# Optimization experiments

Hardware: AMD Instinct MI355X
Metric: run time of the kernel (lower is better)

Reference implementation:

```python
import jax, jax.numpy as jnp
import numpy as np

B = 256          # graphs per batch
N = 128          # nodes per graph (equal-size graphs; batch is block-contiguous)
P = N * (N - 1) // 2  # pairs per graph = 8128
E = B * 1024     # total edges
D = 128          # node feature dim
L = 32           # latent dim

# precomputed local upper-triangular pair indices (constants)
_PI, _PJ = np.triu_indices(N, k=1)
_PI = jnp.asarray(_PI); _PJ = jnp.asarray(_PJ)


def setup_inputs() -> dict:
    key = jax.random.key(0)
    ks = jax.random.split(key, 8)
    x = jax.random.normal(ks[0], (B * N, D), dtype=jnp.float32)
    # within-graph edges with local i < j
    li = jax.random.randint(ks[1], (E,), 0, N - 1)
    r = jax.random.randint(ks[2], (E,), 0, 1 << 30)
    lj = li + 1 + r % (N - 1 - li)
    g = jax.random.randint(ks[3], (E,), 0, B)
    off = g * N
    edge_index = jnp.stack([off + li, off + lj]).astype(jnp.int64)
    batch = jnp.repeat(jnp.arange(B), N).astype(jnp.int64)
    eps = jax.random.normal(ks[4], (B * N, L), dtype=jnp.float32)
    W1 = jax.random.normal(ks[5], (D, D), dtype=jnp.float32) * 0.05
    b1 = jnp.zeros((D,), dtype=jnp.float32)
    Wmu = jax.random.normal(ks[6], (D, L), dtype=jnp.float32) * 0.05
    bmu = jnp.zeros((L,), dtype=jnp.float32)
    Wls = jax.random.normal(ks[7], (D, L), dtype=jnp.float32) * 0.05
    bls = jnp.zeros((L,), dtype=jnp.float32)
    return {"x": x, "edge_index": edge_index, "batch": batch, "eps": eps,
            "W1": W1, "b1": b1, "Wmu": Wmu, "bmu": bmu, "Wls": Wls, "bls": bls}


def reference(x, edge_index, batch, eps, W1, b1, Wmu, bmu, Wls, bls):
    src, dst = edge_index[0], edge_index[1]
    # --- encoder: one symmetric message-passing layer -> Gaussian q per node ---
    agg = jnp.zeros_like(x).at[dst].add(x[src]).at[src].add(x[dst])
    h = jax.nn.relu((x + agg) @ W1 + b1)
    mu = h @ Wmu + bmu                       # [BN, L]
    log_std = h @ Wls + bls
    std = jnp.exp(log_std)
    z = mu + std * eps                       # rsample
    # --- KL(q || N(0,I)) per node, summed per graph (kls[b]) ---
    kl_node = 0.5 * jnp.sum(std * std + mu * mu - 1.0 - 2.0 * log_std, axis=-1)
    kls = jax.ops.segment_sum(kl_node, batch, num_segments=B)  # [B]
    # --- link targets: scatter edges into triangular pair slots ---
    li, lj, be = src % N, dst % N, src // N
    pidx = li * (2 * N - li - 1) // 2 + (lj - li - 1)
    targets = jnp.zeros((B, P), dtype=z.dtype).at[be, pidx].set(1.0)
    # --- inner-product Bernoulli decoder over all pairs of every graph ---
    zb = z.reshape(B, N, L)
    logits = jnp.einsum('bpl,bpl->bp', zb[:, _PI], zb[:, _PJ])   # [B, P]
    log_probs = jnp.sum(targets * logits - jax.nn.softplus(logits), axis=-1)  # [B]
    elbo = jnp.mean(log_probs - kls)
    return -elbo
```

## Files before the change

kernel.cpp:

```cpp
#include <hip/hip_runtime.h>
#include <math.h>

#define B_ 256
#define N_ 128
#define D_ 128
#define L_ 32
#define E_ 262144
#define PW_ 254
#define DCAP 96

#define NDEG_OFF 0
#define BM_OFF   32768
#define KLS_OFF  97792
#define LP_OFF   98048
#define ADJ_OFF  98304
#define Z_OFF    884736
#define ZERO_WORDS 98304

__global__ __launch_bounds__(256) void k_build(
    const int* __restrict__ ei, unsigned* __restrict__ ndeg,
    unsigned char* __restrict__ adj, unsigned* __restrict__ bm)
{
    int e = blockIdx.x * 256 + threadIdx.x;
    int src = ei[e], dst = ei[E_ + e];
    unsigned s1 = atomicAdd(&ndeg[src], 1u);
    if (s1 < DCAP) adj[(size_t)src * DCAP + s1] = (unsigned char)(dst & 127);
    unsigned s2 = atomicAdd(&ndeg[dst], 1u);
    if (s2 < DCAP) adj[(size_t)dst * DCAP + s2] = (unsigned char)(src & 127);
    int li = src & 127, lj = dst & 127, g = src >> 7;
    int p = li * (255 - li) / 2 + (lj - li - 1);
    atomicOr(&bm[g * PW_ + (p >> 5)], 1u << (p & 31));
}

__global__ __launch_bounds__(256, 4) void k_encoder(
    const float* __restrict__ x, const unsigned* __restrict__ ndeg,
    const unsigned char* __restrict__ adj,
    const float* __restrict__ W1, const float* __restrict__ b1,
    const float* __restrict__ Wmu, const float* __restrict__ bmu,
    const float* __restrict__ Wls, const float* __restrict__ bls,
    const float* __restrict__ eps,
    float* __restrict__ z, float* __restrict__ kls)
{
    __shared__ float XAs[32 * 132];
    __shared__ float Ws[4096];
    __shared__ float RED[256];
    int t = threadIdx.x;
    int g = blockIdx.x & 255;
    int quar = blockIdx.x >> 8;
    int row0 = g * 128 + quar * 32;
    int rg = t >> 5;
    int cg = t & 31;

    {
        int nidx = t >> 4;
        int fo = (t & 15) * 8;
        for (int p = 0; p < 2; ++p) {
            int lrow = p * 16 + nidx;
            int gnode = row0 + lrow;
            const float* xr = x + (size_t)gnode * 128 + fo;
            float4 a0 = *(const float4*)xr;
            float4 a1 = *(const float4*)(xr + 4);
            int deg = (int)ndeg[gnode];
            if (deg > DCAP) deg = DCAP;
            const unsigned char* al = adj + (size_t)gnode * DCAP;
            const float* gx = x + (size_t)(gnode & ~127) * 128 + fo;
            int e = 0;
            for (; e + 4 <= deg; e += 4) {
                unsigned pk = *(const unsigned*)(al + e);
                const float* r0 = gx + (pk & 255u) * 128;
                const float* r1 = gx + ((pk >> 8) & 255u) * 128;
                const float* r2 = gx + ((pk >> 16) & 255u) * 128;
                const float* r3 = gx + (pk >> 24) * 128;
                float4 v00 = *(const float4*)r0, v01 = *(const float4*)(r0 + 4);
                float4 v10 = *(const float4*)r1, v11 = *(const float4*)(r1 + 4);
                float4 v20 = *(const float4*)r2, v21 = *(const float4*)(r2 + 4);
                float4 v30 = *(const float4*)r3, v31 = *(const float4*)(r3 + 4);
                a0.x += v00.x + v10.x + v20.x + v30.x;
                a0.y += v00.y + v10.y + v20.y + v30.y;
                a0.z += v00.z + v10.z + v20.z + v30.z;
                a0.w += v00.w + v10.w + v20.w + v30.w;
                a1.x += v01.x + v11.x + v21.x + v31.x;
                a1.y += v01.y + v11.y + v21.y + v31.y;
                a1.z += v01.z + v11.z + v21.z + v31.z;
                a1.w += v01.w + v11.w + v21.w + v31.w;
            }
            for (; e < deg; ++e) {
                const float* r = gx + (unsigned)al[e] * 128;
                float4 v0 = *(const float4*)r, v1 = *(const float4*)(r + 4);
                a0.x += v0.x; a0.y += v0.y; a0.z += v0.z; a0.w += v0.w;
                a1.x += v1.x; a1.y += v1.y; a1.z += v1.z; a1.w += v1.w;
            }
            *(float4*)(XAs + lrow * 132 + fo) = a0;
            *(float4*)(XAs + lrow * 132 + fo + 4) = a1;
        }
    }
    __syncthreads();

    float acc[4][4];
    #pragma unroll
    for (int i = 0; i < 4; ++i)
        #pragma unroll
        for (int j = 0; j < 4; ++j) acc[i][j] = 0.f;

    for (int kq = 0; kq < 4; ++kq) {
        if (kq) __syncthreads();
        #pragma unroll
        for (int i = 0; i < 4; ++i) {
            int c = t + i * 256;
            ((float4*)Ws)[c] = ((const float4*)(W1 + kq * 4096))[c];
        }
        __syncthreads();
        #pragma unroll 2
        for (int k = 0; k < 32; k += 4) {
            float4 av[4], wv[4];
            #pragma unroll
            for (int i = 0; i < 4; ++i)
                av[i] = *(const float4*)(XAs + (4 * rg + i) * 132 + kq * 32 + k);
            #pragma unroll
            for (int dk = 0; dk < 4; ++dk)
                wv[dk] = *(const float4*)(Ws + (k + dk) * 128 + 4 * cg);
            #pragma unroll
            for (int i = 0; i < 4; ++i) {
                acc[i][0] += av[i].x * wv[0].x + av[i].y * wv[1].x + av[i].z * wv[2].x + av[i].w * wv[3].x;
                acc[i][1] += av[i].x * wv[0].y + av[i].y * wv[1].y + av[i].z * wv[2].y + av[i].w * wv[3].y;
                acc[i][2] += av[i].x * wv[0].z + av[i].y * wv[1].z + av[i].z * wv[2].z + av[i].w * wv[3].z;
                acc[i][3] += av[i].x * wv[0].w + av[i].y * wv[1].w + av[i].z * wv[2].w + av[i].w * wv[3].w;
            }
        }
    }
    __syncthreads();

    {
        float4 bb = *(const float4*)(b1 + 4 * cg);
        #pragma unroll
        for (int i = 0; i < 4; ++i) {
            float4 h;
            h.x = fmaxf(acc[i][0] + bb.x, 0.f);
            h.y = fmaxf(acc[i][1] + bb.y, 0.f);
            h.z = fmaxf(acc[i][2] + bb.z, 0.f);
            h.w = fmaxf(acc[i][3] + bb.w, 0.f);
            *(float4*)(XAs + (4 * rg + i) * 132 + 4 * cg) = h;
        }
    }

    float a3[4][2];
    #pragma unroll
    for (int i = 0; i < 4; ++i) { a3[i][0] = 0.f; a3[i][1] = 0.f; }

    for (int kh = 0; kh < 2; ++kh) {
        __syncthreads();
        #pragma unroll
        for (int i = 0; i < 4; ++i) {
            int c = t + i * 256;
            int row = c >> 4, col4 = (c & 15) << 2;
            int rowg = kh * 64 + row;
            float4 v = (col4 < 32) ? *(const float4*)(Wmu + rowg * 32 + col4)
                                   : *(const float4*)(Wls + rowg * 32 + col4 - 32);
            *(float4*)(Ws + row * 64 + col4) = v;
        }
        __syncthreads();
        #pragma unroll 2
        for (int k = 0; k < 64; k += 4) {
            float4 av[4];
            float2 wv[4];
            #pragma unroll
            for (int i = 0; i < 4; ++i)
                av[i] = *(const float4*)(XAs + (4 * rg + i) * 132 + kh * 64 + k);
            #pragma unroll
            for (int dk = 0; dk < 4; ++dk)
                wv[dk] = *(const float2*)(Ws + (k + dk) * 64 + 2 * cg);
            #pragma unroll
            for (int i = 0; i < 4; ++i) {
                a3[i][0] += av[i].x * wv[0].x + av[i].y * wv[1].x + av[i].z * wv[2].x + av[i].w * wv[3].x;
                a3[i][1] += av[i].x * wv[0].y + av[i].y * wv[1].y + av[i].z * wv[2].y + av[i].w * wv[3].y;
            }
        }
    }
    {
        float2 bv = (cg < 16) ? *(const float2*)(bmu + 2 * cg)
                              : *(const float2*)(bls + 2 * cg - 32);
        #pragma unroll
        for (int i = 0; i < 4; ++i) { a3[i][0] += bv.x; a3[i][1] += bv.y; }
    }

    float o3[4][2];
    #pragma unroll
    for (int i = 0; i < 4; ++i) {
        o3[i][0] = __shfl_xor(a3[i][0], 16);
        o3[i][1] = __shfl_xor(a3[i][1], 16);
    }

    float klsum = 0.f;
    if (cg < 16) {
        int lo = cg;
        #pragma unroll
        for (int i = 0; i < 4; ++i) {
            int rowg = row0 + 4 * rg + i;
            float mu0 = a3[i][0], mu1 = a3[i][1];
            float ls0 = o3[i][0], ls1 = o3[i][1];
            float2 ev = *(const float2*)(eps + (size_t)rowg * 32 + 2 * lo);
            float s0 = expf(ls0), s1 = expf(ls1);
            float2 zv = make_float2(mu0 + s0 * ev.x, mu1 + s1 * ev.y);
            *(float2*)(z + (size_t)rowg * 32 + 2 * lo) = zv;
            klsum += s0 * s0 + mu0 * mu0 - 1.f - 2.f * ls0
                   + s1 * s1 + mu1 * mu1 - 1.f - 2.f * ls1;
        }
    }
    RED[t] = klsum;
    __syncthreads();
    for (int s = 128; s > 0; s >>= 1) {
        if (t < s) RED[t] += RED[t + s];
        __syncthreads();
    }
    if (t == 0) atomicAdd(&kls[g], 0.5f * RED[0]);
}

__global__ __launch_bounds__(256) void k_decoder(
    const float* __restrict__ z, const unsigned* __restrict__ bitmap,
    float* __restrict__ logp)
{
    __shared__ float zT[32 * 132];
    __shared__ unsigned bm[PW_];
    __shared__ float RED[256];
    int b = blockIdx.x & 255, quar = blockIdx.x >> 8, t = threadIdx.x;

    #pragma unroll
    for (int i = 0; i < 16; ++i) {
        int c = t + i * 256;
        int n = c >> 5, l = c & 31;
        zT[l * 132 + n] = z[((size_t)b * N_ + n) * L_ + l];
    }
    if (t < PW_) bm[t] = bitmap[b * PW_ + t];
    __syncthreads();

    int i0 = quar * 32 + ((t >> 5) << 2);
    int j0 = (t & 31) << 2;
    float g[4][4];
    #pragma unroll
    for (int a = 0; a < 4; ++a)
        #pragma unroll
        for (int c = 0; c < 4; ++c) g[a][c] = 0.f;

    #pragma unroll 4
    for (int l = 0; l < 32; ++l) {
        float4 a0 = *(const float4*)(zT + l * 132 + i0);
        float4 b0 = *(const float4*)(zT + l * 132 + j0);
        float za[4] = {a0.x, a0.y, a0.z, a0.w};
        float zb[4] = {b0.x, b0.y, b0.z, b0.w};
        #pragma unroll
        for (int a = 0; a < 4; ++a)
            #pragma unroll
            for (int c = 0; c < 4; ++c) g[a][c] += za[a] * zb[c];
    }

    float sum = 0.f;
    #pragma unroll
    for (int a = 0; a < 4; ++a) {
        int i = i0 + a;
        #pragma unroll
        for (int c = 0; c < 4; ++c) {
            int j = j0 + c;
            if (j > i) {
                float lg = g[a][c];
                int p = i * (255 - i) / 2 + (j - i - 1);
                unsigned bit = (bm[p >> 5] >> (p & 31)) & 1u;
                float sp = log1pf(expf(-fabsf(lg))) + fmaxf(lg, 0.f);
                sum += bit ? (lg - sp) : (-sp);
            }
        }
    }
    RED[t] = sum;
    __syncthreads();
    for (int s = 128; s > 0; s >>= 1) {
        if (t < s) RED[t] += RED[t + s];
        __syncthreads();
    }
    if (t == 0) atomicAdd(&logp[b], RED[0]);
}

__global__ __launch_bounds__(256) void k_finalize(
    const float* __restrict__ kls, const float* __restrict__ logp,
    float* __restrict__ out)
{
    __shared__ float RED[256];
    int t = threadIdx.x;
    RED[t] = logp[t] - kls[t];
    __syncthreads();
    for (int s = 128; s > 0; s >>= 1) {
        if (t < s) RED[t] += RED[t + s];
        __syncthreads();
    }
    if (t == 0) out[0] = -RED[0] * (1.0f / 256.0f);
}

extern "C" void kernel_launch(void* const* d_in, const int* in_sizes, int n_in,
                              void* d_out, int out_size, void* d_ws, size_t ws_size,
                              hipStream_t stream) {
    const float* x   = (const float*)d_in[0];
    const int*   ei  = (const int*)d_in[1];
    const float* eps = (const float*)d_in[3];
    const float* W1  = (const float*)d_in[4];
    const float* b1  = (const float*)d_in[5];
    const float* Wmu = (const float*)d_in[6];
    const float* bmu = (const float*)d_in[7];
    const float* Wls = (const float*)d_in[8];
    const float* bls = (const float*)d_in[9];

    unsigned* wsw = (unsigned*)d_ws;
    unsigned*      ndeg = wsw + NDEG_OFF;
    unsigned*      bm   = wsw + BM_OFF;
    float*         kls  = (float*)(wsw + KLS_OFF);
    float*         logp = (float*)(wsw + LP_OFF);
    unsigned char* adj  = (unsigned char*)(wsw + ADJ_OFF);
    float*         z    = (float*)(wsw + Z_OFF);

    hipMemsetAsync(d_ws, 0, ZERO_WORDS * sizeof(unsigned), stream);

    k_build   <<<E_ / 256, 256, 0, stream>>>(ei, ndeg, adj, bm);
    k_encoder <<<1024, 256, 0, stream>>>(x, ndeg, adj, W1, b1, Wmu, bmu,
                                         Wls, bls, eps, z, kls);
    k_decoder <<<4 * B_, 256, 0, stream>>>(z, bm, logp);
    k_finalize<<<1, 256, 0, stream>>>(kls, logp, (float*)d_out);
}
```

Measured before the change: 188.5 us.

## Double-buffer encoder weight tiles, use per-wave rows, fast math, shuffle reductions

The encoder now gives each wave its own 8-row slice of aggregated features. It streams W1 and the mu/log-std weights through double-buffered shared tiles, prefetching the next chunk into registers while computing on the current one, so there are fewer barriers per chunk. Block-level shared-memory tree reductions in the encoder and decoder become wavefront shuffle reductions with one atomic per wave. expf/log1pf are replaced by the __expf/__logf intrinsics, which are cheaper but slightly less accurate, and the per-wave atomics add more atomic traffic.

Measured after the change: 277.8 us. 1.47x slower.

```diff
diff --git a/kernel.cpp b/kernel.cpp
--- a/kernel.cpp
+++ b/kernel.cpp
@@ -41,22 +41,28 @@
     const float* __restrict__ eps,
     float* __restrict__ z, float* __restrict__ kls)
 {
-    __shared__ float XAs[32 * 132];
-    __shared__ float Ws[4096];
-    __shared__ float RED[256];
+    __shared__ float XAW[4][8 * 132];
+    __shared__ float Ws[2][2048];
     int t = threadIdx.x;
     int g = blockIdx.x & 255;
     int quar = blockIdx.x >> 8;
     int row0 = g * 128 + quar * 32;
-    int rg = t >> 5;
-    int cg = t & 31;
+    int w = t >> 6, lane = t & 63;
+    int rg = lane >> 5;
+    int cg = lane & 31;
+    float* myA = XAW[w];
+    int wrow0 = row0 + w * 8;
+
+    float4 wp0 = ((const float4*)W1)[t];
+    float4 wp1 = ((const float4*)W1)[t + 256];
 
     {
-        int nidx = t >> 4;
-        int fo = (t & 15) * 8;
+        int sub = lane >> 4;
+        int fo = (lane & 15) * 8;
+        #pragma unroll 2
         for (int p = 0; p < 2; ++p) {
-            int lrow = p * 16 + nidx;
-            int gnode = row0 + lrow;
+            int lrow = p * 4 + sub;
+            int gnode = wrow0 + lrow;
             const float* xr = x + (size_t)gnode * 128 + fo;
             float4 a0 = *(const float4*)xr;
             float4 a1 = *(const float4*)(xr + 4);
@@ -90,10 +96,12 @@
                 a0.x += v0.x; a0.y += v0.y; a0.z += v0.z; a0.w += v0.w;
                 a1.x += v1.x; a1.y += v1.y; a1.z += v1.z; a1.w += v1.w;
             }
-            *(float4*)(XAs + lrow * 132 + fo) = a0;
-            *(float4*)(XAs + lrow * 132 + fo + 4) = a1;
-        }
-    }
+            *(float4*)(myA + lrow * 132 + fo) = a0;
+            *(float4*)(myA + lrow * 132 + fo + 4) = a1;
+        }
+    }
+    ((float4*)Ws[0])[t] = wp0;
+    ((float4*)Ws[0])[t + 256] = wp1;
     __syncthreads();
 
     float acc[4][4];
@@ -102,23 +110,21 @@
         #pragma unroll
         for (int j = 0; j < 4; ++j) acc[i][j] = 0.f;
 
-    for (int kq = 0; kq < 4; ++kq) {
-        if (kq) __syncthreads();
-        #pragma unroll
-        for (int i = 0; i < 4; ++i) {
-            int c = t + i * 256;
-            ((float4*)Ws)[c] = ((const float4*)(W1 + kq * 4096))[c];
-        }
-        __syncthreads();
-        #pragma unroll 2
-        for (int k = 0; k < 32; k += 4) {
+    for (int c = 0; c < 8; ++c) {
+        if (c < 7) {
+            wp0 = ((const float4*)(W1 + (c + 1) * 2048))[t];
+            wp1 = ((const float4*)(W1 + (c + 1) * 2048))[t + 256];
+        }
+        const float* WsC = Ws[c & 1];
+        #pragma unroll
+        for (int k = 0; k < 16; k += 4) {
             float4 av[4], wv[4];
             #pragma unroll
             for (int i = 0; i < 4; ++i)
-                av[i] = *(const float4*)(XAs + (4 * rg + i) * 132 + kq * 32 + k);
+                av[i] = *(const float4*)(myA + (4 * rg + i) * 132 + c * 16 + k);
             #pragma unroll
             for (int dk = 0; dk < 4; ++dk)
-                wv[dk] = *(const float4*)(Ws + (k + dk) * 128 + 4 * cg);
+                wv[dk] = *(const float4*)(WsC + (k + dk) * 128 + 4 * cg);
             #pragma unroll
             for (int i = 0; i < 4; ++i) {
                 acc[i][0] += av[i].x * wv[0].x + av[i].y * wv[1].x + av[i].z * wv[2].x + av[i].w * wv[3].x;
@@ -127,8 +133,13 @@
                 acc[i][3] += av[i].x * wv[0].w + av[i].y * wv[1].w + av[i].z * wv[2].w + av[i].w * wv[3].w;
             }
         }
-    }
-    __syncthreads();
+        if (c < 7) {
+            float* WsN = Ws[(c + 1) & 1];
+            ((float4*)WsN)[t] = wp0;
+            ((float4*)WsN)[t + 256] = wp1;
+            __syncthreads();
+        }
+    }
 
     {
         float4 bb = *(const float4*)(b1 + 4 * cg);
@@ -139,55 +150,72 @@
             h.y = fmaxf(acc[i][1] + bb.y, 0.f);
             h.z = fmaxf(acc[i][2] + bb.z, 0.f);
             h.w = fmaxf(acc[i][3] + bb.w, 0.f);
-            *(float4*)(XAs + (4 * rg + i) * 132 + 4 * cg) = h;
-        }
-    }
-
-    float a3[4][2];
-    #pragma unroll
-    for (int i = 0; i < 4; ++i) { a3[i][0] = 0.f; a3[i][1] = 0.f; }
-
-    for (int kh = 0; kh < 2; ++kh) {
-        __syncthreads();
-        #pragma unroll
-        for (int i = 0; i < 4; ++i) {
-            int c = t + i * 256;
-            int row = c >> 4, col4 = (c & 15) << 2;
-            int rowg = kh * 64 + row;
-            float4 v = (col4 < 32) ? *(const float4*)(Wmu + rowg * 32 + col4)
-                                   : *(const float4*)(Wls + rowg * 32 + col4 - 32);
-            *(float4*)(Ws + row * 64 + col4) = v;
-        }
-        __syncthreads();
-        #pragma unroll 2
-        for (int k = 0; k < 64; k += 4) {
+            *(float4*)(myA + (4 * rg + i) * 132 + 4 * cg) = h;
+        }
+    }
+
+    {
+        int f0 = t, f1 = t + 256;
+        int r0_ = f0 >> 4, c0_ = (f0 & 15) << 2;
+        int r1_ = f1 >> 4, c1_ = (f1 & 15) << 2;
+        wp0 = (c0_ < 32) ? *(const float4*)(Wmu + r0_ * 32 + c0_)
+                         : *(const float4*)(Wls + r0_ * 32 + c0_ - 32);
+        wp1 = (c1_ < 32) ? *(const float4*)(Wmu + r1_ * 32 + c1_)
+                         : *(const float4*)(Wls + r1_ * 32 + c1_ - 32);
+        ((float4*)Ws[0])[f0] = wp0;
+        ((float4*)Ws[0])[f1] = wp1;
+    }
+    __syncthreads();
+
+    float a2[4][2];
+    #pragma unroll
+    for (int i = 0; i < 4; ++i) { a2[i][0] = 0.f; a2[i][1] = 0.f; }
+
+    for (int q = 0; q < 4; ++q) {
+        if (q < 3) {
+            int f0 = t, f1 = t + 256;
+            int r0_ = (q + 1) * 32 + (f0 >> 4), c0_ = (f0 & 15) << 2;
+            int r1_ = (q + 1) * 32 + (f1 >> 4), c1_ = (f1 & 15) << 2;
+            wp0 = (c0_ < 32) ? *(const float4*)(Wmu + r0_ * 32 + c0_)
+                             : *(const float4*)(Wls + r0_ * 32 + c0_ - 32);
+            wp1 = (c1_ < 32) ? *(const float4*)(Wmu + r1_ * 32 + c1_)
+                             : *(const float4*)(Wls + r1_ * 32 + c1_ - 32);
+        }
+        const float* WsC = Ws[q & 1];
+        #pragma unroll
+        for (int k = 0; k < 32; k += 4) {
             float4 av[4];
             float2 wv[4];
             #pragma unroll
             for (int i = 0; i < 4; ++i)
-                av[i] = *(const float4*)(XAs + (4 * rg + i) * 132 + kh * 64 + k);
+                av[i] = *(const float4*)(myA + (4 * rg + i) * 132 + q * 32 + k);
             #pragma unroll
             for (int dk = 0; dk < 4; ++dk)
-                wv[dk] = *(const float2*)(Ws + (k + dk) * 64 + 2 * cg);
+                wv[dk] = *(const float2*)(WsC + (k + dk) * 64 + 2 * cg);
             #pragma unroll
             for (int i = 0; i < 4; ++i) {
-                a3[i][0] += av[i].x * wv[0].x + av[i].y * wv[1].x + av[i].z * wv[2].x + av[i].w * wv[3].x;
-                a3[i][1] += av[i].x * wv[0].y + av[i].y * wv[1].y + av[i].z * wv[2].y + av[i].w * wv[3].y;
-            }
+                a2[i][0] += av[i].x * wv[0].x + av[i].y * wv[1].x + av[i].z * wv[2].x + av[i].w * wv[3].x;
+                a2[i][1] += av[i].x * wv[0].y + av[i].y * wv[1].y + av[i].z * wv[2].y + av[i].w * wv[3].y;
+            }
+        }
+        if (q < 3) {
+            float* WsN = Ws[(q + 1) & 1];
+            ((float4*)WsN)[t] = wp0;
+            ((float4*)WsN)[t + 256] = wp1;
+            __syncthreads();
         }
     }
     {
-        float2 bv = (cg < 16) ? *(const float2*)(bmu + 2 * cg)
-                              : *(const float2*)(bls + 2 * cg - 32);
-        #pragma unroll
-        for (int i = 0; i < 4; ++i) { a3[i][0] += bv.x; a3[i][1] += bv.y; }
-    }
-
-    float o3[4][2];
+        float2 bv = (cg < 16) ? ((const float2*)bmu)[cg] : ((const float2*)bls)[cg - 16];
+        #pragma unroll
+        for (int i = 0; i < 4; ++i) { a2[i][0] += bv.x; a2[i][1] += bv.y; }
+    }
+
+    float o2[4][2];
     #pragma unroll
     for (int i = 0; i < 4; ++i) {
-        o3[i][0] = __shfl_xor(a3[i][0], 16);
-        o3[i][1] = __shfl_xor(a3[i][1], 16);
+        o2[i][0] = __shfl_xor(a2[i][0], 16);
+        o2[i][1] = __shfl_xor(a2[i][1], 16);
     }
 
     float klsum = 0.f;
@@ -195,24 +223,20 @@
         int lo = cg;
         #pragma unroll
         for (int i = 0; i < 4; ++i) {
-            int rowg = row0 + 4 * rg + i;
-            float mu0 = a3[i][0], mu1 = a3[i][1];
-            float ls0 = o3[i][0], ls1 = o3[i][1];
+            int rowg = wrow0 + 4 * rg + i;
+            float mu0 = a2[i][0], mu1 = a2[i][1];
+            float ls0 = o2[i][0], ls1 = o2[i][1];
             float2 ev = *(const float2*)(eps + (size_t)rowg * 32 + 2 * lo);
-            float s0 = expf(ls0), s1 = expf(ls1);
+            float s0 = __expf(ls0), s1 = __expf(ls1);
             float2 zv = make_float2(mu0 + s0 * ev.x, mu1 + s1 * ev.y);
             *(float2*)(z + (size_t)rowg * 32 + 2 * lo) = zv;
             klsum += s0 * s0 + mu0 * mu0 - 1.f - 2.f * ls0
                    + s1 * s1 + mu1 * mu1 - 1.f - 2.f * ls1;
         }
     }
-    RED[t] = klsum;
-    __syncthreads();
-    for (int s = 128; s > 0; s >>= 1) {
-        if (t < s) RED[t] += RED[t + s];
-        __syncthreads();
-    }
-    if (t == 0) atomicAdd(&kls[g], 0.5f * RED[0]);
+    #pragma unroll
+    for (int off = 32; off > 0; off >>= 1) klsum += __shfl_xor(klsum, off);
+    if (lane == 0) atomicAdd(&kls[g], 0.5f * klsum);
 }
 
 __global__ __launch_bounds__(256) void k_decoder(
@@ -221,7 +245,6 @@
 {
     __shared__ float zT[32 * 132];
     __shared__ unsigned bm[PW_];
-    __shared__ float RED[256];
     int b = blockIdx.x & 255, quar = blockIdx.x >> 8, t = threadIdx.x;
 
     #pragma unroll
@@ -264,18 +287,14 @@
                 float lg = g[a][c];
                 int p = i * (255 - i) / 2 + (j - i - 1);
                 unsigned bit = (bm[p >> 5] >> (p & 31)) & 1u;
-                float sp = log1pf(expf(-fabsf(lg))) + fmaxf(lg, 0.f);
+                float sp = __logf(1.f + __expf(-fabsf(lg))) + fmaxf(lg, 0.f);
                 sum += bit ? (lg - sp) : (-sp);
             }
         }
     }
-    RED[t] = sum;
-    __syncthreads();
-    for (int s = 128; s > 0; s >>= 1) {
-        if (t < s) RED[t] += RED[t + s];
-        __syncthreads();
-    }
-    if (t == 0) atomicAdd(&logp[b], RED[0]);
+    #pragma unroll
+    for (int off = 32; off > 0; off >>= 1) sum += __shfl_xor(sum, off);
+    if ((t & 63) == 0) atomicAdd(&logp[b], sum);
 }
 
 __global__ __launch_bounds__(256) void k_finalize(
```
